# Kernel optimization log

Measured on AMD Instinct MI355X. Metric: run time of the kernel, lower is better.

## Reference

```python
import jax, jax.numpy as jnp
import numpy as np

B, T, E, H = 8, 2048, 1024, 64

def setup_inputs() -> dict:
    key = jax.random.key(0)
    kx, kq, kk, kv = jax.random.split(key, 4)
    x = jax.random.normal(kx, (B, T, E), dtype=jnp.float32)
    # torch Linear(E, H, bias=False): weight [H, E]; store transposed [E, H]
    scale = 1.0 / np.sqrt(E)
    Wq = jax.random.uniform(kq, (E, H), dtype=jnp.float32, minval=-scale, maxval=scale)
    Wk = jax.random.uniform(kk, (E, H), dtype=jnp.float32, minval=-scale, maxval=scale)
    Wv = jax.random.uniform(kv, (E, H), dtype=jnp.float32, minval=-scale, maxval=scale)
    return {"x": x, "Wq": Wq, "Wk": Wk, "Wv": Wv}

def reference(x, Wq, Wk, Wv):
    # x: [B,T,E]
    q = x @ Wq  # [B,T,H]
    k = x @ Wk
    v = x @ Wv
    head_size = q.shape[-1]
    scores = jnp.einsum('bth,bsh->bts', q, k) * (head_size ** -0.5)  # [B,T,T]
    Tlen = x.shape[1]
    causal = jnp.tril(jnp.ones((Tlen, Tlen), dtype=bool))
    scores = jnp.where(causal, scores, -jnp.inf)
    weights = jax.nn.softmax(scores, axis=-1)
    # dropout p=0.0 -> identity
    out = jnp.einsum('bts,bsh->bth', weights, v)  # [B,T,H]
    return out
```

## Files before the change

kernel.cpp:

```cpp
#include <hip/hip_runtime.h>
#include <hip/hip_bf16.h>

#define B_  8
#define T_  2048
#define E_  1024
#define H_  64
#define BT_ (B_*T_)

typedef __attribute__((ext_vector_type(8))) __bf16 bf16x8;
typedef __attribute__((ext_vector_type(4))) float  f32x4;

__device__ __forceinline__ unsigned short f2bfu(float f) {
    union { float f; unsigned u; } v; v.f = f;
    unsigned r = v.u + 0x7fffu + ((v.u >> 16) & 1u);
    return (unsigned short)(r >> 16);
}

#define QSCALE (0.125f * 1.44269504f)

__global__ __launch_bounds__(256)
void wprep_kernel(const float* __restrict__ Wq,
                  const float* __restrict__ Wk,
                  const float* __restrict__ Wv,
                  unsigned short* __restrict__ wf)
{
    const int c = blockIdx.x / 3;
    const int m = blockIdx.x % 3;
    const float* W = (m == 0) ? Wq : (m == 1 ? Wk : Wv);
    const float scale = (m == 0) ? QSCALE : 1.0f;

    const int n    = threadIdx.x >> 6;
    const int lane = threadIdx.x & 63;
    const int quad = lane >> 4;
    const int col  = lane & 15;
    const int h    = n * 16 + col;

    unsigned short tmp[8];
#pragma unroll
    for (int j = 0; j < 8; ++j)
        tmp[j] = f2bfu(W[(c * 32 + quad * 8 + j) * H_ + h] * scale);
    *(uint4*)&wf[(((c * 3 + m) * 4 + n) * 64 + lane) * 8] = *(uint4*)tmp;
}

__global__ __launch_bounds__(256, 4)
void qkv_kernel(const float* __restrict__ x,
                const unsigned short* __restrict__ wf,
                unsigned short* __restrict__ qb,
                unsigned short* __restrict__ kb,
                unsigned short* __restrict__ vtb)
{
    const int tid  = threadIdx.x;
    const int wave = tid >> 6;
    const int lane = tid & 63;
    const int quad = lane >> 4;
    const int col  = lane & 15;
    const long r0  = (long)blockIdx.x * 16;

    f32x4 acc[3];
#pragma unroll
    for (int m = 0; m < 3; ++m) acc[m] = (f32x4){0.f, 0.f, 0.f, 0.f};

    const float* xb = x + (r0 + col) * E_ + quad * 8;

    float4 a0 = *(const float4*)xb;
    float4 a1 = *(const float4*)(xb + 4);

#pragma unroll 4
    for (int c = 0; c < 32; ++c) {
        float4 n0 = a0, n1 = a1;
        if (c + 1 < 32) {
            n0 = *(const float4*)(xb + (c + 1) * 32);
            n1 = *(const float4*)(xb + (c + 1) * 32 + 4);
        }
        unsigned pk[4];
        pk[0] = f2bfu(a0.x) | ((unsigned)f2bfu(a0.y) << 16);
        pk[1] = f2bfu(a0.z) | ((unsigned)f2bfu(a0.w) << 16);
        pk[2] = f2bfu(a1.x) | ((unsigned)f2bfu(a1.y) << 16);
        pk[3] = f2bfu(a1.z) | ((unsigned)f2bfu(a1.w) << 16);
        bf16x8 af = *(bf16x8*)pk;
#pragma unroll
        for (int m = 0; m < 3; ++m) {
            bf16x8 bfg = *(const bf16x8*)&wf[(((c * 3 + m) * 4 + wave) * 64 + lane) * 8];
            acc[m] = __builtin_amdgcn_mfma_f32_16x16x32_bf16(af, bfg, acc[m], 0, 0, 0);
        }
        a0 = n0; a1 = n1;
    }

    const int bidx = (int)(r0 >> 11);
    const int h    = wave * 16 + col;
#pragma unroll
    for (int r = 0; r < 4; ++r) {
        long t = r0 + quad * 4 + r;
        qb[t * H_ + h] = f2bfu(acc[0][r]);
        kb[t * H_ + h] = f2bfu(acc[1][r]);
        vtb[((long)(bidx * H_ + h)) * T_ + (t & (T_ - 1))] = f2bfu(acc[2][r]);
    }
}

#define PSS 72

__global__ __launch_bounds__(512, 4)
void attn_kernel(const unsigned short* __restrict__ qb,
                 const unsigned short* __restrict__ kb,
                 const unsigned short* __restrict__ vtb,
                 float* __restrict__ out)
{
    __shared__ unsigned short ps[8][16 * PSS];
    __shared__ float oc[8][16][68];
    __shared__ float ml[8][2][16];

    const int tid  = threadIdx.x;
    const int g    = tid >> 6;
    const int lane = tid & 63;
    const int quad = lane >> 4;
    const int col  = lane & 15;
    const int b    = blockIdx.x & 7;
    const int p    = blockIdx.x >> 3;

    const unsigned short* qbb = qb  + (long)b * T_ * H_;
    const unsigned short* kbb = kb  + (long)b * T_ * H_;
    const unsigned short* vbb = vtb + (long)b * H_ * T_;

    for (int half = 0; half < 2; ++half) {
        const int qt = half ? (127 - p) : p;
        const int nt = (qt + 4) >> 2;

        bf16x8 qa0 = *(const bf16x8*)&qbb[(qt * 16 + col) * H_ + quad * 8];
        bf16x8 qa1 = *(const bf16x8*)&qbb[(qt * 16 + col) * H_ + 32 + quad * 8];

        f32x4 o[4];
        float m_i[4], l_i[4];
#pragma unroll
        for (int n = 0; n < 4; ++n) o[n] = (f32x4){0.f, 0.f, 0.f, 0.f};
#pragma unroll
        for (int r = 0; r < 4; ++r) { m_i[r] = -1e30f; l_i[r] = 0.f; }

        for (int s = g; s < nt; s += 8) {
            f32x4 sa[4];
#pragma unroll
            for (int kt = 0; kt < 4; ++kt) {
                const unsigned short* kp = kbb + ((long)(s * 64 + kt * 16 + col)) * H_ + quad * 8;
                bf16x8 kf0 = *(const bf16x8*)kp;
                bf16x8 kf1 = *(const bf16x8*)(kp + 32);
                sa[kt] = (f32x4){0.f, 0.f, 0.f, 0.f};
                sa[kt] = __builtin_amdgcn_mfma_f32_16x16x32_bf16(qa0, kf0, sa[kt], 0, 0, 0);
                sa[kt] = __builtin_amdgcn_mfma_f32_16x16x32_bf16(qa1, kf1, sa[kt], 0, 0, 0);
            }

            if (s == nt - 1) {
#pragma unroll
                for (int kt = 0; kt < 4; ++kt) {
                    int kg = s * 64 + kt * 16 + col;
#pragma unroll
                    for (int r = 0; r < 4; ++r) {
                        int qg = qt * 16 + quad * 4 + r;
                        if (kg > qg) sa[kt][r] = -1e30f;
                    }
                }
            }

            float mx[4];
#pragma unroll
            for (int r = 0; r < 4; ++r)
                mx[r] = fmaxf(fmaxf(sa[0][r], sa[1][r]), fmaxf(sa[2][r], sa[3][r]));
#pragma unroll
            for (int off = 1; off < 16; off <<= 1)
#pragma unroll
                for (int r = 0; r < 4; ++r)
                    mx[r] = fmaxf(mx[r], __shfl_xor(mx[r], off, 64));

            float alpha[4], mnew[4];
#pragma unroll
            for (int r = 0; r < 4; ++r) {
                mnew[r]  = fmaxf(m_i[r], mx[r]);
                alpha[r] = __builtin_amdgcn_exp2f(m_i[r] - mnew[r]);
                m_i[r]   = mnew[r];
            }

            float rs[4] = {0.f, 0.f, 0.f, 0.f};
#pragma unroll
            for (int kt = 0; kt < 4; ++kt)
#pragma unroll
                for (int r = 0; r < 4; ++r) {
                    float pv = __builtin_amdgcn_exp2f(sa[kt][r] - mnew[r]);
                    rs[r] += pv;
                    ps[g][(quad * 4 + r) * PSS + kt * 16 + col] = f2bfu(pv);
                }
#pragma unroll
            for (int off = 1; off < 16; off <<= 1)
#pragma unroll
                for (int r = 0; r < 4; ++r)
                    rs[r] += __shfl_xor(rs[r], off, 64);
#pragma unroll
            for (int r = 0; r < 4; ++r)
                l_i[r] = l_i[r] * alpha[r] + rs[r];

#pragma unroll
            for (int n = 0; n < 4; ++n)
#pragma unroll
                for (int r = 0; r < 4; ++r)
                    o[n][r] *= alpha[r];

            bf16x8 pa0 = *(const bf16x8*)&ps[g][col * PSS + quad * 8];
            bf16x8 pa1 = *(const bf16x8*)&ps[g][col * PSS + 32 + quad * 8];
#pragma unroll
            for (int n = 0; n < 4; ++n) {
                const unsigned short* vp = vbb + ((long)(n * 16 + col)) * T_ + s * 64 + quad * 8;
                bf16x8 vf0 = *(const bf16x8*)vp;
                bf16x8 vf1 = *(const bf16x8*)(vp + 32);
                o[n] = __builtin_amdgcn_mfma_f32_16x16x32_bf16(pa0, vf0, o[n], 0, 0, 0);
                o[n] = __builtin_amdgcn_mfma_f32_16x16x32_bf16(pa1, vf1, o[n], 0, 0, 0);
            }
        }

#pragma unroll
        for (int r = 0; r < 4; ++r) {
            int row = quad * 4 + r;
#pragma unroll
            for (int n = 0; n < 4; ++n)
                oc[g][row][n * 16 + col] = o[n][r];
        }
        if (col == 0) {
#pragma unroll
            for (int r = 0; r < 4; ++r) {
                ml[g][0][quad * 4 + r] = m_i[r];
                ml[g][1][quad * 4 + r] = l_i[r];
            }
        }
        __syncthreads();

#pragma unroll
        for (int rr = 0; rr < 2; ++rr) {
            int row = g * 2 + rr;
            float M = ml[0][0][row];
#pragma unroll
            for (int j = 1; j < 8; ++j) M = fmaxf(M, ml[j][0][row]);
            float lsum = 0.f, osum = 0.f;
#pragma unroll
            for (int j = 0; j < 8; ++j) {
                float wgt = __builtin_amdgcn_exp2f(ml[j][0][row] - M);
                lsum += ml[j][1][row] * wgt;
                osum += oc[j][row][lane] * wgt;
            }
            out[((long)b * T_ + qt * 16 + row) * H_ + lane] = osum / lsum;
        }
        __syncthreads();
    }
}

extern "C" void kernel_launch(void* const* d_in, const int* in_sizes, int n_in,
                              void* d_out, int out_size, void* d_ws, size_t ws_size,
                              hipStream_t stream) {
    (void)in_sizes; (void)n_in; (void)out_size; (void)ws_size;
    const float* x  = (const float*)d_in[0];
    const float* Wq = (const float*)d_in[1];
    const float* Wk = (const float*)d_in[2];
    const float* Wv = (const float*)d_in[3];

    unsigned short* qb  = (unsigned short*)d_ws;
    unsigned short* kb  = qb + (size_t)BT_ * H_;
    unsigned short* vtb = kb + (size_t)BT_ * H_;
    unsigned short* wf  = vtb + (size_t)BT_ * H_;

    wprep_kernel<<<96, 256, 0, stream>>>(Wq, Wk, Wv, wf);
    qkv_kernel<<<BT_ / 16, 256, 0, stream>>>(x, wf, qb, kb, vtb);
    attn_kernel<<<B_ * 64, 512, 0, stream>>>(qb, kb, vtb, (float*)d_out);
}
```

Baseline: 170.9 us.

## Prefetch x/W and K tiles into registers, alias shared buffers, relax launch bounds

In the projection kernel, x is now loaded four steps ahead and the packed weight fragments two steps ahead in register ring buffers, and bf16 packing uses the hardware conversion intrinsic. In the attention kernel, the K fragments for the next tile are prefetched while the current scores are computed. The P staging buffer is aliased with the output-combine buffer to cut shared memory, with an extra barrier added before reuse. The launch bound occupancy hint drops from 4 to 2, which allows more registers per thread at the cost of fewer resident waves.

```diff
diff --git a/kernel.cpp b/kernel.cpp
--- a/kernel.cpp
+++ b/kernel.cpp
@@ -14,6 +14,12 @@
     union { float f; unsigned u; } v; v.f = f;
     unsigned r = v.u + 0x7fffu + ((v.u >> 16) & 1u);
     return (unsigned short)(r >> 16);
+}
+
+__device__ __forceinline__ unsigned pk2(float lo, float hi) {
+    __hip_bfloat162 h = __float22bfloat162_rn(float2{lo, hi});
+    union { __hip_bfloat162 h; unsigned u; } v; v.h = h;
+    return v.u;
 }
 
 #define QSCALE (0.125f * 1.44269504f)
@@ -62,28 +68,43 @@
 
     const float* xb = x + (r0 + col) * E_ + quad * 8;
 
-    float4 a0 = *(const float4*)xb;
-    float4 a1 = *(const float4*)(xb + 4);
-
-#pragma unroll 4
+    float4 ax[4][2];
+#pragma unroll
+    for (int d = 0; d < 4; ++d) {
+        ax[d][0] = *(const float4*)(xb + d * 32);
+        ax[d][1] = *(const float4*)(xb + d * 32 + 4);
+    }
+    bf16x8 bw[2][3];
+#pragma unroll
+    for (int d = 0; d < 2; ++d)
+#pragma unroll
+        for (int m = 0; m < 3; ++m)
+            bw[d][m] = *(const bf16x8*)&wf[(((d * 3 + m) * 4 + wave) * 64 + lane) * 8];
+
     for (int c = 0; c < 32; ++c) {
-        float4 n0 = a0, n1 = a1;
-        if (c + 1 < 32) {
-            n0 = *(const float4*)(xb + (c + 1) * 32);
-            n1 = *(const float4*)(xb + (c + 1) * 32 + 4);
-        }
+        float4 a0 = ax[c & 3][0], a1 = ax[c & 3][1];
+        bf16x8 b0 = bw[c & 1][0], b1 = bw[c & 1][1], b2 = bw[c & 1][2];
+
+        if (c + 4 < 32) {
+            ax[c & 3][0] = *(const float4*)(xb + (c + 4) * 32);
+            ax[c & 3][1] = *(const float4*)(xb + (c + 4) * 32 + 4);
+        }
+        if (c + 2 < 32) {
+#pragma unroll
+            for (int m = 0; m < 3; ++m)
+                bw[c & 1][m] = *(const bf16x8*)&wf[((((c + 2) * 3 + m) * 4 + wave) * 64 + lane) * 8];
+        }
+
         unsigned pk[4];
-        pk[0] = f2bfu(a0.x) | ((unsigned)f2bfu(a0.y) << 16);
-        pk[1] = f2bfu(a0.z) | ((unsigned)f2bfu(a0.w) << 16);
-        pk[2] = f2bfu(a1.x) | ((unsigned)f2bfu(a1.y) << 16);
-        pk[3] = f2bfu(a1.z) | ((unsigned)f2bfu(a1.w) << 16);
+        pk[0] = pk2(a0.x, a0.y);
+        pk[1] = pk2(a0.z, a0.w);
+        pk[2] = pk2(a1.x, a1.y);
+        pk[3] = pk2(a1.z, a1.w);
         bf16x8 af = *(bf16x8*)pk;
-#pragma unroll
-        for (int m = 0; m < 3; ++m) {
-            bf16x8 bfg = *(const bf16x8*)&wf[(((c * 3 + m) * 4 + wave) * 64 + lane) * 8];
-            acc[m] = __builtin_amdgcn_mfma_f32_16x16x32_bf16(af, bfg, acc[m], 0, 0, 0);
-        }
-        a0 = n0; a1 = n1;
+
+        acc[0] = __builtin_amdgcn_mfma_f32_16x16x32_bf16(af, b0, acc[0], 0, 0, 0);
+        acc[1] = __builtin_amdgcn_mfma_f32_16x16x32_bf16(af, b1, acc[1], 0, 0, 0);
+        acc[2] = __builtin_amdgcn_mfma_f32_16x16x32_bf16(af, b2, acc[2], 0, 0, 0);
     }
 
     const int bidx = (int)(r0 >> 11);
@@ -99,15 +120,16 @@
 
 #define PSS 72
 
-__global__ __launch_bounds__(512, 4)
+__global__ __launch_bounds__(512, 2)
 void attn_kernel(const unsigned short* __restrict__ qb,
                  const unsigned short* __restrict__ kb,
                  const unsigned short* __restrict__ vtb,
                  float* __restrict__ out)
 {
-    __shared__ unsigned short ps[8][16 * PSS];
-    __shared__ float oc[8][16][68];
-    __shared__ float ml[8][2][16];
+    __shared__ char smem[8 * 16 * 68 * 4 + 8 * 2 * 16 * 4];
+    unsigned short* ps = (unsigned short*)smem;
+    float* oc = (float*)smem;
+    float* ml = (float*)(smem + 8 * 16 * 68 * 4);
 
     const int tid  = threadIdx.x;
     const int g    = tid >> 6;
@@ -135,16 +157,32 @@
 #pragma unroll
         for (int r = 0; r < 4; ++r) { m_i[r] = -1e30f; l_i[r] = 0.f; }
 
+        bf16x8 kf[8];
+        if (g < nt) {
+#pragma unroll
+            for (int kt = 0; kt < 4; ++kt) {
+                const unsigned short* kp = kbb + ((long)(g * 64 + kt * 16 + col)) * H_ + quad * 8;
+                kf[kt * 2]     = *(const bf16x8*)kp;
+                kf[kt * 2 + 1] = *(const bf16x8*)(kp + 32);
+            }
+        }
+
         for (int s = g; s < nt; s += 8) {
             f32x4 sa[4];
 #pragma unroll
             for (int kt = 0; kt < 4; ++kt) {
-                const unsigned short* kp = kbb + ((long)(s * 64 + kt * 16 + col)) * H_ + quad * 8;
-                bf16x8 kf0 = *(const bf16x8*)kp;
-                bf16x8 kf1 = *(const bf16x8*)(kp + 32);
                 sa[kt] = (f32x4){0.f, 0.f, 0.f, 0.f};
-                sa[kt] = __builtin_amdgcn_mfma_f32_16x16x32_bf16(qa0, kf0, sa[kt], 0, 0, 0);
-                sa[kt] = __builtin_amdgcn_mfma_f32_16x16x32_bf16(qa1, kf1, sa[kt], 0, 0, 0);
+                sa[kt] = __builtin_amdgcn_mfma_f32_16x16x32_bf16(qa0, kf[kt * 2],     sa[kt], 0, 0, 0);
+                sa[kt] = __builtin_amdgcn_mfma_f32_16x16x32_bf16(qa1, kf[kt * 2 + 1], sa[kt], 0, 0, 0);
+            }
+
+            if (s + 8 < nt) {
+#pragma unroll
+                for (int kt = 0; kt < 4; ++kt) {
+                    const unsigned short* kp = kbb + ((long)((s + 8) * 64 + kt * 16 + col)) * H_ + quad * 8;
+                    kf[kt * 2]     = *(const bf16x8*)kp;
+                    kf[kt * 2 + 1] = *(const bf16x8*)(kp + 32);
+                }
             }
 
             if (s == nt - 1) {
@@ -184,7 +222,7 @@
                 for (int r = 0; r < 4; ++r) {
                     float pv = __builtin_amdgcn_exp2f(sa[kt][r] - mnew[r]);
                     rs[r] += pv;
-                    ps[g][(quad * 4 + r) * PSS + kt * 16 + col] = f2bfu(pv);
+                    ps[g * 16 * PSS + (quad * 4 + r) * PSS + kt * 16 + col] = f2bfu(pv);
                 }
 #pragma unroll
             for (int off = 1; off < 16; off <<= 1)
@@ -201,8 +239,8 @@
                 for (int r = 0; r < 4; ++r)
                     o[n][r] *= alpha[r];
 
-            bf16x8 pa0 = *(const bf16x8*)&ps[g][col * PSS + quad * 8];
-            bf16x8 pa1 = *(const bf16x8*)&ps[g][col * PSS + 32 + quad * 8];
+            bf16x8 pa0 = *(const bf16x8*)&ps[g * 16 * PSS + col * PSS + quad * 8];
+            bf16x8 pa1 = *(const bf16x8*)&ps[g * 16 * PSS + col * PSS + 32 + quad * 8];
 #pragma unroll
             for (int n = 0; n < 4; ++n) {
                 const unsigned short* vp = vbb + ((long)(n * 16 + col)) * T_ + s * 64 + quad * 8;
@@ -213,18 +251,19 @@
             }
         }
 
+        __syncthreads();
 #pragma unroll
         for (int r = 0; r < 4; ++r) {
             int row = quad * 4 + r;
 #pragma unroll
             for (int n = 0; n < 4; ++n)
-                oc[g][row][n * 16 + col] = o[n][r];
+                oc[(g * 16 + row) * 68 + n * 16 + col] = o[n][r];
         }
         if (col == 0) {
 #pragma unroll
             for (int r = 0; r < 4; ++r) {
-                ml[g][0][quad * 4 + r] = m_i[r];
-                ml[g][1][quad * 4 + r] = l_i[r];
+                ml[(g * 2 + 0) * 16 + quad * 4 + r] = m_i[r];
+                ml[(g * 2 + 1) * 16 + quad * 4 + r] = l_i[r];
             }
         }
         __syncthreads();
@@ -232,15 +271,15 @@
 #pragma unroll
         for (int rr = 0; rr < 2; ++rr) {
             int row = g * 2 + rr;
-            float M = ml[0][0][row];
-#pragma unroll
-            for (int j = 1; j < 8; ++j) M = fmaxf(M, ml[j][0][row]);
+            float M = ml[0 * 32 + row];
+#pragma unroll
+            for (int j = 1; j < 8; ++j) M = fmaxf(M, ml[j * 32 + row]);
             float lsum = 0.f, osum = 0.f;
 #pragma unroll
             for (int j = 0; j < 8; ++j) {
-                float wgt = __builtin_amdgcn_exp2f(ml[j][0][row] - M);
-                lsum += ml[j][1][row] * wgt;
-                osum += oc[j][row][lane] * wgt;
+                float wgt = __builtin_amdgcn_exp2f(ml[j * 32 + row] - M);
+                lsum += ml[j * 32 + 16 + row] * wgt;
+                osum += oc[(j * 16 + row) * 68 + lane] * wgt;
             }
             out[((long)b * T_ + qt * 16 + row) * H_ + lane] = osum / lsum;
         }
```

Result: no change. 170.1 us (-0.5%).
